# Kernel optimization log

Measured on AMD Instinct MI355X. Metric: run time of the kernel, lower is better.

Reference implementation:

```python
import jax, jax.numpy as jnp
import numpy as np

B, N, D, P = 64, 1024, 256, 256


def setup_inputs() -> dict:
    key = jax.random.key(0)
    kx, k1, k2, k4 = jax.random.split(key, 4)
    x = jax.random.normal(kx, (B, N, D), dtype=jnp.float32)
    # weights ~ random_uniform(-0.05, 0.05) in the original; scale here is irrelevant for math
    w1 = jax.random.uniform(k1, (D, P), dtype=jnp.float32, minval=-0.05, maxval=0.05)
    w2 = jax.random.uniform(k2, (D, P), dtype=jnp.float32, minval=-0.05, maxval=0.05)
    w4 = jax.random.uniform(k4, (P, 1), dtype=jnp.float32, minval=-0.05, maxval=0.05)
    return {"x": x, "w1": w1, "w2": w2, "w4": w4}


def reference(x, w1, w2, w4):
    # x: [B, N, D] (already stacked/transposed; query_n=key_n=values=x in the original)
    q = jax.nn.sigmoid(jnp.einsum('bnd,dp->bnp', x, w1))  # [B,N,P]
    k = jax.nn.sigmoid(jnp.einsum('bnd,dp->bnp', x, w2))  # [B,N,P]
    temper = jnp.sqrt(jnp.asarray(w1.shape[1], x.dtype))
    attn = jax.nn.softmax(jnp.einsum('bnp,bmp->bnm', q, k) / temper, axis=2)  # [B,N,N]
    # dropout(0.1) in the original is inference-identity here
    out = jnp.einsum('bnm,bmd->bnd', attn, x)             # [B,N,D]
    a = jax.nn.softmax(jnp.einsum('bnd,do->bno', out, w4), axis=1)  # [B,N,1]
    sentence = jnp.sum(x * a, axis=1)                     # [B,D]
    return sentence
```

## Files before the change

### kernel.cpp

```cpp
#include <hip/hip_runtime.h>
#include <cstdint>
#include <cstddef>

constexpr int BB = 64;
constexpr int NN = 1024;
constexpr int DD = 256;
constexpr int PP = 256;

typedef short short8 __attribute__((ext_vector_type(8)));
typedef float f32x4 __attribute__((ext_vector_type(4)));

__device__ __forceinline__ unsigned short f2bf(float f) {
    union { float f; uint32_t u; } v; v.f = f;
    uint32_t u = v.u;
    uint32_t r = (u + 0x7FFFu + ((u >> 16) & 1u)) >> 16;
    return (unsigned short)r;
}

__device__ __forceinline__ void async_load16(void* lds, const void* g) {
    __builtin_amdgcn_global_load_lds(
        (const __attribute__((address_space(1))) unsigned int*)g,
        (__attribute__((address_space(3))) unsigned int*)lds, 16, 0, 0);
}

__device__ __forceinline__ void stage_tile(const unsigned short* src_base,
                                           unsigned short* lds, int wv, int lane) {
    const char* base = (const char*)src_base;
    char* dst0 = (char*)lds + wv * 8192;
    #pragma unroll
    for (int i = 0; i < 8; i++) {
        int row = wv * 16 + i * 2 + (lane >> 5);
        int blk = (lane & 31) ^ (row & 7);
        async_load16(dst0 + i * 1024, base + row * 512 + blk * 16);
    }
}

__device__ __forceinline__ void stage32(const unsigned short* base,
                                        unsigned short* lds, int wv, int lane) {
    char* dst0 = (char*)lds + wv * 4096;
    #pragma unroll
    for (int i = 0; i < 4; i++) {
        int row = wv * 8 + i * 2 + (lane >> 5);
        int blk = (lane & 31) ^ (row & 7);
        async_load16(dst0 + i * 1024, (const char*)base + row * 512 + blk * 16);
    }
}

__device__ __forceinline__ short8 lds_frag(const unsigned short* lds, int row, int kidx) {
    uint32_t byte = (uint32_t)(row * 512) + (uint32_t)(((kidx ^ (row & 7)) & 31) << 4);
    return *reinterpret_cast<const short8*>(reinterpret_cast<const char*>(lds) + byte);
}

__global__ void prep_wt(const float* __restrict__ w1, const float* __restrict__ w2,
                        unsigned short* __restrict__ wt) {
    int j = blockIdx.x;
    int d = threadIdx.x;
    const float* w = (j < PP) ? w1 : w2;
    int jj = j & (PP - 1);
    wt[j * DD + d] = f2bf(w[d * PP + jj]);
}

__global__ __launch_bounds__(256) void qk_fused(const float* __restrict__ x,
                                                const unsigned short* __restrict__ wt,
                                                const float* __restrict__ w4,
                                                unsigned short* __restrict__ qb,
                                                unsigned short* __restrict__ kb,
                                                float* __restrict__ xv) {
    __shared__ __align__(16) unsigned short wtile[2][16384];
    const int t = threadIdx.x, wv = t >> 6, lane = t & 63, l15 = lane & 15, l4 = lane >> 4;
    const int rowBase = blockIdx.x * 128 + wv * 32;

    stage_tile(wt, wtile[0], wv, lane);

    short8 xf[2][8];
    float xvp[2] = {0.f, 0.f};
    #pragma unroll
    for (int kc = 0; kc < 8; kc++) {
        float4 w4a = *reinterpret_cast<const float4*>(w4 + kc * 32 + l4 * 8);
        float4 w4b = *reinterpret_cast<const float4*>(w4 + kc * 32 + l4 * 8 + 4);
        #pragma unroll
        for (int s = 0; s < 2; s++) {
            const float* xr = x + (size_t)(rowBase + s * 16 + l15) * DD + kc * 32 + l4 * 8;
            float4 a = *reinterpret_cast<const float4*>(xr);
            float4 b = *reinterpret_cast<const float4*>(xr + 4);
            xvp[s] += a.x * w4a.x + a.y * w4a.y + a.z * w4a.z + a.w * w4a.w
                    + b.x * w4b.x + b.y * w4b.y + b.z * w4b.z + b.w * w4b.w;
            short8 f;
            f[0] = (short)f2bf(a.x); f[1] = (short)f2bf(a.y);
            f[2] = (short)f2bf(a.z); f[3] = (short)f2bf(a.w);
            f[4] = (short)f2bf(b.x); f[5] = (short)f2bf(b.y);
            f[6] = (short)f2bf(b.z); f[7] = (short)f2bf(b.w);
            xf[s][kc] = f;
        }
    }
    #pragma unroll
    for (int s = 0; s < 2; s++) {
        xvp[s] += __shfl_xor(xvp[s], 16);
        xvp[s] += __shfl_xor(xvp[s], 32);
        if (l4 == 0) xv[rowBase + s * 16 + l15] = xvp[s];
    }

    __syncthreads();
    int buf = 0;
    for (int ct = 0; ct < 8; ct++) {
        if (ct + 1 < 8) stage_tile(wt + (size_t)(ct + 1) * 64 * DD, wtile[buf ^ 1], wv, lane);
        unsigned short* outp = (ct < 4) ? qb : kb;
        const int pc0 = (ct & 3) * 64;
        #pragma unroll
        for (int st = 0; st < 4; st++) {
            f32x4 acc0 = {0.f, 0.f, 0.f, 0.f};
            f32x4 acc1 = {0.f, 0.f, 0.f, 0.f};
            #pragma unroll
            for (int kc = 0; kc < 8; kc++) {
                short8 wf = lds_frag(wtile[buf], st * 16 + l15, kc * 4 + l4);
                acc0 = __builtin_amdgcn_mfma_f32_16x16x32_bf16(wf, xf[0][kc], acc0, 0, 0, 0);
                acc1 = __builtin_amdgcn_mfma_f32_16x16x32_bf16(wf, xf[1][kc], acc1, 0, 0, 0);
            }
            const int pc = pc0 + st * 16 + l4 * 4;
            ushort4 pk;
            pk.x = f2bf(1.f / (1.f + __expf(-acc0[0])));
            pk.y = f2bf(1.f / (1.f + __expf(-acc0[1])));
            pk.z = f2bf(1.f / (1.f + __expf(-acc0[2])));
            pk.w = f2bf(1.f / (1.f + __expf(-acc0[3])));
            *reinterpret_cast<ushort4*>(outp + (size_t)(rowBase + l15) * PP + pc) = pk;
            pk.x = f2bf(1.f / (1.f + __expf(-acc1[0])));
            pk.y = f2bf(1.f / (1.f + __expf(-acc1[1])));
            pk.z = f2bf(1.f / (1.f + __expf(-acc1[2])));
            pk.w = f2bf(1.f / (1.f + __expf(-acc1[3])));
            *reinterpret_cast<ushort4*>(outp + (size_t)(rowBase + 16 + l15) * PP + pc) = pk;
        }
        __syncthreads();
        buf ^= 1;
    }
}

__global__ __launch_bounds__(256, 4) void attn_logit(const unsigned short* __restrict__ qb,
                                                     const unsigned short* __restrict__ kb,
                                                     const float* __restrict__ xv,
                                                     float* __restrict__ numo,
                                                     float* __restrict__ deno) {
    __shared__ __align__(16) unsigned short kt[2][8192];
    __shared__ float xvs[512];
    const int qt = blockIdx.x >> 1, half = blockIdx.x & 1, b = blockIdx.y;
    const int t = threadIdx.x, wv = t >> 6, lane = t & 63, l15 = lane & 15, l4 = lane >> 4;
    const unsigned short* kbb = kb + ((size_t)b * NN + half * 512) * PP;

    stage32(kbb, kt[0], wv, lane);

    xvs[t] = xv[b * NN + half * 512 + t];
    xvs[t + 256] = xv[b * NN + half * 512 + t + 256];

    short8 qf[2][8];
    const int qrow0 = b * NN + qt * 128 + wv * 32;
    #pragma unroll
    for (int s = 0; s < 2; s++) {
        const unsigned short* qrow = qb + (size_t)(qrow0 + s * 16 + l15) * PP;
        #pragma unroll
        for (int kc = 0; kc < 8; kc++)
            qf[s][kc] = *reinterpret_cast<const short8*>(qrow + kc * 32 + l4 * 8);
    }

    float den[2][4], num[2][4];
    #pragma unroll
    for (int s = 0; s < 2; s++)
        #pragma unroll
        for (int r = 0; r < 4; r++) { den[s][r] = 0.f; num[s][r] = 0.f; }

    __syncthreads();
    int buf = 0;
    for (int mc = 0; mc < 16; mc++) {
        if (mc + 1 < 16) stage32(kbb + (size_t)(mc + 1) * 32 * PP, kt[buf ^ 1], wv, lane);
        #pragma unroll
        for (int st = 0; st < 2; st++) {
            f32x4 a0 = {0.f, 0.f, 0.f, 0.f};
            f32x4 a1 = {0.f, 0.f, 0.f, 0.f};
            #pragma unroll
            for (int kc = 0; kc < 8; kc++) {
                short8 kf = lds_frag(kt[buf], st * 16 + l15, kc * 4 + l4);
                a0 = __builtin_amdgcn_mfma_f32_16x16x32_bf16(qf[0][kc], kf, a0, 0, 0, 0);
                a1 = __builtin_amdgcn_mfma_f32_16x16x32_bf16(qf[1][kc], kf, a1, 0, 0, 0);
            }
            float xvv = xvs[mc * 32 + st * 16 + l15];
            #pragma unroll
            for (int r = 0; r < 4; r++) {
                float e0 = __expf(a0[r] * 0.0625f);
                den[0][r] += e0; num[0][r] += e0 * xvv;
                float e1 = __expf(a1[r] * 0.0625f);
                den[1][r] += e1; num[1][r] += e1 * xvv;
            }
        }
        __syncthreads();
        buf ^= 1;
    }
    #pragma unroll
    for (int s = 0; s < 2; s++)
        #pragma unroll
        for (int r = 0; r < 4; r++) {
            #pragma unroll
            for (int off = 1; off < 16; off <<= 1) {
                den[s][r] += __shfl_xor(den[s][r], off);
                num[s][r] += __shfl_xor(num[s][r], off);
            }
        }
    if (l15 == 0) {
        #pragma unroll
        for (int s = 0; s < 2; s++)
            #pragma unroll
            for (int r = 0; r < 4; r++) {
                int n = qt * 128 + wv * 32 + s * 16 + l4 * 4 + r;
                size_t o = (size_t)half * BB * NN + (size_t)b * NN + n;
                numo[o] = num[s][r];
                deno[o] = den[s][r];
            }
    }
}

__global__ __launch_bounds__(256) void sent_partial(const float* __restrict__ x,
                                                    const float* __restrict__ numo,
                                                    const float* __restrict__ deno,
                                                    float* __restrict__ part) {
    __shared__ float al[64];
    __shared__ float redA[4];
    __shared__ float redB[4];
    const int b = blockIdx.x, ch = blockIdx.y;
    const int t = threadIdx.x;
    float l[4];
    #pragma unroll
    for (int i = 0; i < 4; i++) {
        int n = b * NN + t + i * 256;
        l[i] = (numo[n] + numo[BB * NN + n]) / (deno[n] + deno[BB * NN + n]);
    }
    float mx = fmaxf(fmaxf(l[0], l[1]), fmaxf(l[2], l[3]));
    #pragma unroll
    for (int off = 1; off < 64; off <<= 1) mx = fmaxf(mx, __shfl_xor(mx, off));
    if ((t & 63) == 0) redA[t >> 6] = mx;
    __syncthreads();
    mx = fmaxf(fmaxf(redA[0], redA[1]), fmaxf(redA[2], redA[3]));
    float e[4], es = 0.f;
    #pragma unroll
    for (int i = 0; i < 4; i++) { e[i] = __expf(l[i] - mx); es += e[i]; }
    #pragma unroll
    for (int off = 1; off < 64; off <<= 1) es += __shfl_xor(es, off);
    if ((t & 63) == 0) redB[t >> 6] = es;
    __syncthreads();
    float inv = 1.f / (redB[0] + redB[1] + redB[2] + redB[3]);
    int ei = ch >> 2;
    float sel = (ei == 0) ? e[0] : (ei == 1) ? e[1] : (ei == 2) ? e[2] : e[3];
    if ((t >> 6) == (ch & 3)) al[t & 63] = sel * inv;
    __syncthreads();
    float acc = 0.f;
    const float* xb = x + ((size_t)b * NN + ch * 64) * DD + t;
    #pragma unroll 8
    for (int n = 0; n < 64; n++)
        acc += al[n] * xb[(size_t)n * DD];
    part[(b * 16 + ch) * DD + t] = acc;
}

__global__ void sent_final(const float* __restrict__ part, float* __restrict__ out) {
    int b = blockIdx.x, t = threadIdx.x;
    float s = 0.f;
    #pragma unroll
    for (int c = 0; c < 16; c++) s += part[(b * 16 + c) * DD + t];
    out[b * DD + t] = s;
}

extern "C" void kernel_launch(void* const* d_in, const int* in_sizes, int n_in,
                              void* d_out, int out_size, void* d_ws, size_t ws_size,
                              hipStream_t stream) {
    (void)in_sizes; (void)n_in; (void)out_size; (void)ws_size;
    const float* x  = (const float*)d_in[0];
    const float* w1 = (const float*)d_in[1];
    const float* w2 = (const float*)d_in[2];
    const float* w4 = (const float*)d_in[3];
    float* out = (float*)d_out;

    char* ws = (char*)d_ws;
    const size_t MB = 1024 * 1024;
    unsigned short* qb   = (unsigned short*)(ws);
    unsigned short* kb   = (unsigned short*)(ws + 32 * MB);
    unsigned short* wt   = (unsigned short*)(ws + 64 * MB);
    float*          xv   = (float*)(ws + 64 * MB + 256 * 1024);
    float*          num  = (float*)(ws + 64 * MB + 512 * 1024);
    float*          den  = (float*)(ws + 64 * MB + 1024 * 1024);
    float*          part = (float*)(ws);

    prep_wt<<<dim3(2 * PP), dim3(DD), 0, stream>>>(w1, w2, wt);
    qk_fused<<<dim3(BB * NN / 128), dim3(256), 0, stream>>>(x, wt, w4, qb, kb, xv);
    attn_logit<<<dim3(16, BB), dim3(256), 0, stream>>>(qb, kb, xv, num, den);
    sent_partial<<<dim3(BB, 16), dim3(256), 0, stream>>>(x, num, den, part);
    sent_final<<<dim3(BB), dim3(DD), 0, stream>>>(part, out);
}
```

Measured before the change: 107.1 us.

## Split attention key range into quarters and shrink QK weight tiles

The attention-logit kernel now splits the key dimension into four quarters instead of two, doubling the grid to 2048 blocks with batch as the fast grid index. It drops the 4-blocks-per-CU launch bound, and the sentence kernel sums four partial numerator/denominator sets. The QK projection kernel stages 32-row weight tiles (half the LDS) over 16 iterations instead of 64-row tiles over 8. bf16 conversion now uses the HIP intrinsic. These changes aim for more parallelism and occupancy, at the cost of more partial writes and reads and more loop iterations and barriers.

```diff
diff --git a/kernel.cpp b/kernel.cpp
--- a/kernel.cpp
+++ b/kernel.cpp
@@ -1,4 +1,5 @@
 #include <hip/hip_runtime.h>
+#include <hip/hip_bf16.h>
 #include <cstdint>
 #include <cstddef>
 
@@ -11,28 +12,15 @@
 typedef float f32x4 __attribute__((ext_vector_type(4)));
 
 __device__ __forceinline__ unsigned short f2bf(float f) {
-    union { float f; uint32_t u; } v; v.f = f;
-    uint32_t u = v.u;
-    uint32_t r = (u + 0x7FFFu + ((u >> 16) & 1u)) >> 16;
-    return (unsigned short)r;
+    union { __hip_bfloat16 h; unsigned short u; } v;
+    v.h = __float2bfloat16(f);
+    return v.u;
 }
 
 __device__ __forceinline__ void async_load16(void* lds, const void* g) {
     __builtin_amdgcn_global_load_lds(
         (const __attribute__((address_space(1))) unsigned int*)g,
         (__attribute__((address_space(3))) unsigned int*)lds, 16, 0, 0);
-}
-
-__device__ __forceinline__ void stage_tile(const unsigned short* src_base,
-                                           unsigned short* lds, int wv, int lane) {
-    const char* base = (const char*)src_base;
-    char* dst0 = (char*)lds + wv * 8192;
-    #pragma unroll
-    for (int i = 0; i < 8; i++) {
-        int row = wv * 16 + i * 2 + (lane >> 5);
-        int blk = (lane & 31) ^ (row & 7);
-        async_load16(dst0 + i * 1024, base + row * 512 + blk * 16);
-    }
 }
 
 __device__ __forceinline__ void stage32(const unsigned short* base,
@@ -66,11 +54,11 @@
                                                 unsigned short* __restrict__ qb,
                                                 unsigned short* __restrict__ kb,
                                                 float* __restrict__ xv) {
-    __shared__ __align__(16) unsigned short wtile[2][16384];
+    __shared__ __align__(16) unsigned short wtile[2][8192];
     const int t = threadIdx.x, wv = t >> 6, lane = t & 63, l15 = lane & 15, l4 = lane >> 4;
     const int rowBase = blockIdx.x * 128 + wv * 32;
 
-    stage_tile(wt, wtile[0], wv, lane);
+    stage32(wt, wtile[0], wv, lane);
 
     short8 xf[2][8];
     float xvp[2] = {0.f, 0.f};
@@ -102,12 +90,12 @@
 
     __syncthreads();
     int buf = 0;
-    for (int ct = 0; ct < 8; ct++) {
-        if (ct + 1 < 8) stage_tile(wt + (size_t)(ct + 1) * 64 * DD, wtile[buf ^ 1], wv, lane);
-        unsigned short* outp = (ct < 4) ? qb : kb;
-        const int pc0 = (ct & 3) * 64;
-        #pragma unroll
-        for (int st = 0; st < 4; st++) {
+    for (int ct = 0; ct < 16; ct++) {
+        if (ct + 1 < 16) stage32(wt + (size_t)(ct + 1) * 32 * DD, wtile[buf ^ 1], wv, lane);
+        unsigned short* outp = (ct < 8) ? qb : kb;
+        const int pc0 = (ct & 7) * 32;
+        #pragma unroll
+        for (int st = 0; st < 2; st++) {
             f32x4 acc0 = {0.f, 0.f, 0.f, 0.f};
             f32x4 acc1 = {0.f, 0.f, 0.f, 0.f};
             #pragma unroll
@@ -134,21 +122,21 @@
     }
 }
 
-__global__ __launch_bounds__(256, 4) void attn_logit(const unsigned short* __restrict__ qb,
-                                                     const unsigned short* __restrict__ kb,
-                                                     const float* __restrict__ xv,
-                                                     float* __restrict__ numo,
-                                                     float* __restrict__ deno) {
+__global__ __launch_bounds__(256) void attn_logit(const unsigned short* __restrict__ qb,
+                                                  const unsigned short* __restrict__ kb,
+                                                  const float* __restrict__ xv,
+                                                  float* __restrict__ numo,
+                                                  float* __restrict__ deno) {
     __shared__ __align__(16) unsigned short kt[2][8192];
-    __shared__ float xvs[512];
-    const int qt = blockIdx.x >> 1, half = blockIdx.x & 1, b = blockIdx.y;
+    __shared__ float xvs[256];
+    const int b = blockIdx.x;
+    const int qt = blockIdx.y >> 2, quarter = blockIdx.y & 3;
     const int t = threadIdx.x, wv = t >> 6, lane = t & 63, l15 = lane & 15, l4 = lane >> 4;
-    const unsigned short* kbb = kb + ((size_t)b * NN + half * 512) * PP;
+    const unsigned short* kbb = kb + ((size_t)b * NN + quarter * 256) * PP;
 
     stage32(kbb, kt[0], wv, lane);
 
-    xvs[t] = xv[b * NN + half * 512 + t];
-    xvs[t + 256] = xv[b * NN + half * 512 + t + 256];
+    xvs[t] = xv[b * NN + quarter * 256 + t];
 
     short8 qf[2][8];
     const int qrow0 = b * NN + qt * 128 + wv * 32;
@@ -168,8 +156,8 @@
 
     __syncthreads();
     int buf = 0;
-    for (int mc = 0; mc < 16; mc++) {
-        if (mc + 1 < 16) stage32(kbb + (size_t)(mc + 1) * 32 * PP, kt[buf ^ 1], wv, lane);
+    for (int mc = 0; mc < 8; mc++) {
+        if (mc + 1 < 8) stage32(kbb + (size_t)(mc + 1) * 32 * PP, kt[buf ^ 1], wv, lane);
         #pragma unroll
         for (int st = 0; st < 2; st++) {
             f32x4 a0 = {0.f, 0.f, 0.f, 0.f};
@@ -208,7 +196,7 @@
             #pragma unroll
             for (int r = 0; r < 4; r++) {
                 int n = qt * 128 + wv * 32 + s * 16 + l4 * 4 + r;
-                size_t o = (size_t)half * BB * NN + (size_t)b * NN + n;
+                size_t o = (size_t)quarter * BB * NN + (size_t)b * NN + n;
                 numo[o] = num[s][r];
                 deno[o] = den[s][r];
             }
@@ -228,7 +216,13 @@
     #pragma unroll
     for (int i = 0; i < 4; i++) {
         int n = b * NN + t + i * 256;
-        l[i] = (numo[n] + numo[BB * NN + n]) / (deno[n] + deno[BB * NN + n]);
+        float ns = 0.f, ds = 0.f;
+        #pragma unroll
+        for (int q = 0; q < 4; q++) {
+            ns += numo[(size_t)q * BB * NN + n];
+            ds += deno[(size_t)q * BB * NN + n];
+        }
+        l[i] = ns / ds;
     }
     float mx = fmaxf(fmaxf(l[0], l[1]), fmaxf(l[2], l[3]));
     #pragma unroll
@@ -281,12 +275,12 @@
     unsigned short* wt   = (unsigned short*)(ws + 64 * MB);
     float*          xv   = (float*)(ws + 64 * MB + 256 * 1024);
     float*          num  = (float*)(ws + 64 * MB + 512 * 1024);
-    float*          den  = (float*)(ws + 64 * MB + 1024 * 1024);
+    float*          den  = (float*)(ws + 64 * MB + 1536 * 1024);
     float*          part = (float*)(ws);
 
     prep_wt<<<dim3(2 * PP), dim3(DD), 0, stream>>>(w1, w2, wt);
     qk_fused<<<dim3(BB * NN / 128), dim3(256), 0, stream>>>(x, wt, w4, qb, kb, xv);
-    attn_logit<<<dim3(16, BB), dim3(256), 0, stream>>>(qb, kb, xv, num, den);
+    attn_logit<<<dim3(BB, 32), dim3(256), 0, stream>>>(qb, kb, xv, num, den);
     sent_partial<<<dim3(BB, 16), dim3(256), 0, stream>>>(x, num, den, part);
     sent_final<<<dim3(BB), dim3(DD), 0, stream>>>(part, out);
 }
```

New measurement: 129.3 us. 20.7% more time.
